# Kernel tuning notes

Measured on AMD Instinct MI355X. Metric: run time of the kernel, lower is better.

The kernel has to match this reference:

```python
import jax, jax.numpy as jnp
import numpy as np

H = 512        # hidden_dim
D_IN = 512     # input_dim
N_ACT = 16     # output_dim
DICT = 8192    # dict_len (episodic memory slots)
B = 4096       # batch
N_CYCLES = 10  # LCA iterations
DT_T = 0.6     # LCA dt/tau
EPS = 1e-8     # cosine-similarity eps


def setup_inputs() -> dict:
    key = jax.random.key(0)
    ks = jax.random.split(key, 12)
    NHT = 4 * H + 3  # (N_VSIG+1)*H + N_SSIG
    s = lambda i, shape, sc=1.0: jax.random.normal(ks[i], shape, jnp.float32) * sc
    return {
        "x_t": s(0, (1, B, D_IN)),
        "h_prev": s(1, (1, B, H), 0.1),
        "c_prev": s(2, (1, B, H), 0.1),
        "W_i2h": s(3, (NHT, D_IN), 1.0 / np.sqrt(D_IN)),
        "b_i2h": jnp.zeros((NHT,), jnp.float32),
        "W_h2h": s(4, (NHT, H), 1.0 / np.sqrt(H)),
        "b_h2h": jnp.zeros((NHT,), jnp.float32),
        "vals": s(5, (DICT, H), 0.1),  # episodic memory table
        "W_ih": s(6, (H, H), 1.0 / np.sqrt(H)),
        "b_ih": jnp.zeros((H,), jnp.float32),
        "W_actor": s(7, (N_ACT, H), 1.0 / np.sqrt(H)),
        "b_actor": jnp.zeros((N_ACT,), jnp.float32),
        "W_critic": s(8, (1, H), 1.0 / np.sqrt(H)),
        "b_critic": jnp.zeros((1,), jnp.float32),
        "mem_ptr": 0,
    }


def _lca(sim, leak, comp, w_input):
    # Leaky competing accumulator over memory slots; sim:[B,DICT], scalars:[B,1]
    ff = w_input * sim
    def step(V, _):
        inhib = comp * (jnp.sum(V, axis=-1, keepdims=True) - V)  # lateral inhibition (excl. self)
        V = jax.nn.relu(V + DT_T * (ff - leak * V - inhib))
        return V, None
    V, _ = jax.lax.scan(step, jnp.zeros_like(sim), None, length=N_CYCLES)
    return V


def reference(x_t, h_prev, c_prev, W_i2h, b_i2h, W_h2h, b_h2h, vals,
              W_ih, b_ih, W_actor, b_actor, W_critic, b_critic, mem_ptr):
    x, h, c = x_t[0], h_prev[0], c_prev[0]  # [B, dim]
    preact = x @ W_i2h.T + b_i2h + h @ W_h2h.T + b_h2h  # [B, 4H+3]
    gates = jax.nn.sigmoid(preact[:, :3 * H])
    f_t = gates[:, :H]
    o_t = gates[:, H:2 * H]
    i_t = gates[:, 2 * H:3 * H]
    inps = jax.nn.sigmoid(preact[:, 3 * H + 0])[:, None]  # input strength (gain=1)
    leak = jax.nn.sigmoid(preact[:, 3 * H + 1])[:, None]
    comp = jax.nn.sigmoid(preact[:, 3 * H + 2])[:, None]
    c_new = jnp.tanh(preact[:, 3 * H + 3:])
    c_t = c * f_t + i_t * c_new
    # --- recall: cosine similarity vs memory, then LCA competition ---
    qn = jnp.linalg.norm(c_t, axis=-1, keepdims=True)        # [B,1]
    mn = jnp.linalg.norm(vals, axis=-1, keepdims=True)       # [DICT,1]
    sim = (c_t @ vals.T) / jnp.maximum(qn * mn.T, EPS)       # [B,DICT]
    w = _lca(sim, leak, comp, inps)                          # [B,DICT]
    m_t = w @ vals                                           # [B,H]
    cm_t = c_t + m_t
    # --- encode: ring-buffer scatter write of cm_t into memory ---
    idx = (mem_ptr + jnp.arange(B)) % DICT
    new_vals = vals.at[idx].set(cm_t)
    h_t = o_t * jnp.tanh(cm_t)
    # --- A2C head ---
    a2c_h = jax.nn.relu(h_t @ W_ih.T + b_ih)
    pi = jax.nn.softmax(a2c_h @ W_actor.T + b_actor, axis=-1)
    value = a2c_h @ W_critic.T + b_critic
    return pi, value, h_t, cm_t, m_t, new_vals
```

## Files before the change

### kernel.cpp

```cpp
#include <hip/hip_runtime.h>
#include <hip/hip_fp16.h>
#include <math.h>

#define HH    512
#define DICT  8192
#define BATCH 4096
#define NCYC  10
#define DTT   0.6f

#define BM  128
#define BKT 64

using f16x8 = __attribute__((ext_vector_type(8))) _Float16;
using f32x4 = __attribute__((ext_vector_type(4))) float;

__device__ __forceinline__ float sigmoidf_(float x) { return 1.0f / (1.0f + __expf(-x)); }

__device__ __forceinline__ float waveReduceSum(float v) {
#pragma unroll
  for (int o = 1; o < 64; o <<= 1) v += __shfl_xor(v, o);
  return v;
}

__device__ __forceinline__ void gld16(const void* g, void* l) {
  __builtin_amdgcn_global_load_lds(
      (const __attribute__((address_space(1))) void*)g,
      (__attribute__((address_space(3))) void*)l, 16, 0, 0);
}

template<int N> __device__ __forceinline__ void vmwait() {
  if constexpr (N == 8)      asm volatile("s_waitcnt vmcnt(8)" ::: "memory");
  else if constexpr (N == 6) asm volatile("s_waitcnt vmcnt(6)" ::: "memory");
  else if constexpr (N == 4) asm volatile("s_waitcnt vmcnt(4)" ::: "memory");
  else if constexpr (N == 3) asm volatile("s_waitcnt vmcnt(3)" ::: "memory");
  else                       asm volatile("s_waitcnt vmcnt(0)" ::: "memory");
  __builtin_amdgcn_sched_barrier(0);
}

__device__ __forceinline__ void blockbar() {
  asm volatile("" ::: "memory");
  __builtin_amdgcn_s_barrier();
  __builtin_amdgcn_sched_barrier(0);
}

template<int ROWS>
__device__ __forceinline__ void stage_tile(const __half* gbase, int ld, char* lds, int tid) {
  constexpr int ISS = ROWS * 8 / 256;
#pragma unroll
  for (int i = 0; i < ISS; ++i) {
    int cidx = i * 256 + tid;
    int row  = cidx >> 3;
    int slot = cidx & 7;
    int k4   = slot ^ (row & 7);
    gld16(gbase + (size_t)row * ld + k4 * 8, lds + cidx * 16);
  }
}

__device__ __forceinline__ f16x8 frag_ld(const char* lds, int row, int kchunk) {
  int slot = kchunk ^ (row & 7);
  return *(const f16x8*)(lds + row * 128 + slot * 16);
}

template<int FN>
__device__ __forceinline__ void tile_mfma(const char* As, const char* Bs,
                                          int lane, int wr, int wc, f32x4 (&acc)[4][FN]) {
  const int g = lane >> 4, r = lane & 15;
#pragma unroll
  for (int ks = 0; ks < 2; ++ks) {
    f16x8 af[4], bfr[FN];
#pragma unroll
    for (int i = 0; i < 4; ++i)
      af[i] = frag_ld(As, wr * 64 + i * 16 + r, ks * 4 + g);
#pragma unroll
    for (int j = 0; j < FN; ++j)
      bfr[j] = frag_ld(Bs, wc * (FN * 16) + j * 16 + r, ks * 4 + g);
#pragma unroll
    for (int i = 0; i < 4; ++i)
#pragma unroll
      for (int j = 0; j < FN; ++j)
        acc[i][j] = __builtin_amdgcn_mfma_f32_16x16x32_f16(af[i], bfr[j], acc[i][j], 0, 0, 0);
  }
}

template<int BN, int FN>
__device__ __forceinline__ void gemm_seg(const __half* A, int lda, const __half* B, int ldb,
                                         int m0, int n0, int K, char* lds, int tid,
                                         f32x4 (&acc)[4][FN]) {
  constexpr int ABYTES = BM * BKT * 2;
  constexpr int BBYTES = BN * BKT * 2;
  constexpr int BUF = ABYTES + BBYTES;
  constexpr int NL = (BM + BN) * 8 / 256;
  const int lane = tid & 63, wid = tid >> 6;
  const int wr = wid >> 1, wc = wid & 1;
  const int nt = K / BKT;
  const __half* Ab = A + (size_t)m0 * lda;
  const __half* Bb = B + (size_t)n0 * ldb;
  stage_tile<BM>(Ab, lda, lds, tid);
  stage_tile<BN>(Bb, ldb, lds + ABYTES, tid);
  int cur = 0;
  for (int t = 0; t < nt; ++t) {
    char* curb = lds + cur * BUF;
    if (t + 1 < nt) {
      char* nxt = lds + (cur ^ 1) * BUF;
      stage_tile<BM>(Ab + (t + 1) * BKT, lda, nxt, tid);
      stage_tile<BN>(Bb + (t + 1) * BKT, ldb, nxt + ABYTES, tid);
      vmwait<NL>();
    } else {
      vmwait<0>();
    }
    blockbar();
    tile_mfma<FN>(curb, curb + ABYTES, lane, wr, wc, acc);
    blockbar();
    cur ^= 1;
  }
}

__device__ __forceinline__ void zero_acc4(f32x4 (&a)[4][4]) {
  f32x4 z = {0.f, 0.f, 0.f, 0.f};
#pragma unroll
  for (int i = 0; i < 4; ++i)
#pragma unroll
    for (int j = 0; j < 4; ++j) a[i][j] = z;
}
__device__ __forceinline__ void zero_acc2(f32x4 (&a)[4][2]) {
  f32x4 z = {0.f, 0.f, 0.f, 0.f};
#pragma unroll
  for (int i = 0; i < 4; ++i)
#pragma unroll
    for (int j = 0; j < 2; ++j) a[i][j] = z;
}

__device__ __forceinline__ int swz32(int row, int k) {
  return k ^ (row & 3) ^ ((row >> 2) & 3);
}

template<int ROWS, int NT>
__device__ __forceinline__ void stage32(const __half* gbase, int ld, char* lds, int tid) {
  constexpr int ISS = ROWS * 4 / NT;
#pragma unroll
  for (int i = 0; i < ISS; ++i) {
    int cidx = i * NT + tid;
    int row  = cidx >> 2;
    int slot = cidx & 3;
    int k4   = swz32(row, slot);
    gld16(gbase + (size_t)row * ld + k4 * 8, lds + cidx * 16);
  }
}

__device__ __forceinline__ f16x8 frag32(const char* lds, int row, int g) {
  int slot = swz32(row, g);
  return *(const f16x8*)(lds + row * 64 + slot * 16);
}

template<int MF, int NF>
__device__ __forceinline__ void tile_mfma32(const char* As, const char* Bs,
                                            int arow0, int brow0, int lane,
                                            f32x4 (&acc)[MF][NF]) {
  const int g = lane >> 4, r = lane & 15;
  f16x8 af[MF], bf[NF];
#pragma unroll
  for (int i = 0; i < MF; ++i) af[i] = frag32(As, arow0 + i * 16 + r, g);
#pragma unroll
  for (int j = 0; j < NF; ++j) bf[j] = frag32(Bs, brow0 + j * 16 + r, g);
#pragma unroll
  for (int i = 0; i < MF; ++i)
#pragma unroll
    for (int j = 0; j < NF; ++j)
      acc[i][j] = __builtin_amdgcn_mfma_f32_16x16x32_f16(af[i], bf[j], acc[i][j], 0, 0, 0);
}

__global__ __launch_bounds__(256) void k_prep(
    const float* __restrict__ x, const float* __restrict__ h,
    const float* __restrict__ Wi, const float* __restrict__ Wh, const float* __restrict__ Wih,
    const float* __restrict__ vals, const int* __restrict__ mptr,
    __half* __restrict__ x_h, __half* __restrict__ h_h,
    __half* __restrict__ Wip_h, __half* __restrict__ Whp_h, __half* __restrict__ Wih_h,
    float* __restrict__ nv, __half* __restrict__ vals_h, float* __restrict__ rmn,
    __half* __restrict__ vT) {
  __shared__ float tile[32][33];
  const int bid = blockIdx.x;
  if (bid < 6400) {
    int gq = bid * 256 + threadIdx.x;
    const float* src; __half* dst; int si, di;
    if (gq < 524288) {
      src = x; dst = x_h; si = di = gq * 4;
    } else if (gq < 1048576) {
      src = h; dst = h_h; si = di = (gq - 524288) * 4;
    } else if (gq < 1310720) {
      int iq = gq - 1048576;
      int jp = iq >> 7, k4 = (iq & 127) << 2;
      int U = jp >> 6, g = (jp >> 4) & 3, r = jp & 15;
      int u = U * 16 + r;
      int orig = g * 512 + u + (g == 3 ? 3 : 0);
      src = Wi; dst = Wip_h; si = orig * 512 + k4; di = jp * 512 + k4;
    } else if (gq < 1572864) {
      int iq = gq - 1310720;
      int jp = iq >> 7, k4 = (iq & 127) << 2;
      int U = jp >> 6, g = (jp >> 4) & 3, r = jp & 15;
      int u = U * 16 + r;
      int orig = g * 512 + u + (g == 3 ? 3 : 0);
      src = Wh; dst = Whp_h; si = orig * 512 + k4; di = jp * 512 + k4;
    } else if (gq < 1638400) {
      int iq = gq - 1572864;
      src = Wih; dst = Wih_h; si = di = iq * 4;
    } else return;
    float4 v = *(const float4*)(src + si);
    *(__half2*)(dst + di)     = __floats2half2_rn(v.x, v.y);
    *(__half2*)(dst + di + 2) = __floats2half2_rn(v.z, v.w);
  } else if (bid < 8448) {
    const int row  = (bid - 6400) * 4 + (threadIdx.x >> 6);
    const int lane = threadIdx.x & 63;
    const float* vr = vals + (size_t)row * HH + lane * 8;
    float4 a = *(const float4*)(vr);
    float4 b = *(const float4*)(vr + 4);
    if (((row + DICT - mptr[0]) & (DICT - 1)) >= BATCH) {
      float* nvp = nv + (size_t)row * HH + lane * 8;
      *(float4*)(nvp)     = a;
      *(float4*)(nvp + 4) = b;
    }
    __half* vh = vals_h + (size_t)row * HH + lane * 8;
    *(__half2*)(vh)     = __floats2half2_rn(a.x, a.y);
    *(__half2*)(vh + 2) = __floats2half2_rn(a.z, a.w);
    *(__half2*)(vh + 4) = __floats2half2_rn(b.x, b.y);
    *(__half2*)(vh + 6) = __floats2half2_rn(b.z, b.w);
    float ss = a.x * a.x + a.y * a.y + a.z * a.z + a.w * a.w
             + b.x * b.x + b.y * b.y + b.z * b.z + b.w * b.w;
    ss = waveReduceSum(ss);
    if (lane == 0) rmn[row] = 1.f / fmaxf(sqrtf(ss), 1e-12f);
  } else {
    const int idx = bid - 8448;
    const int r0 = (idx & 255) * 32, c0 = (idx >> 8) * 32;
    const int tr = threadIdx.x >> 5, tc = threadIdx.x & 31;
#pragma unroll
    for (int p = 0; p < 4; ++p)
      tile[tr + p * 8][tc] = vals[(size_t)(r0 + tr + p * 8) * HH + c0 + tc];
    __syncthreads();
#pragma unroll
    for (int p = 0; p < 4; ++p)
      vT[(size_t)(c0 + tr + p * 8) * DICT + r0 + tc] = __float2half(tile[tc][tr + p * 8]);
  }
}

__global__ __launch_bounds__(256) void k_preact(
    const __half* __restrict__ x_h, const __half* __restrict__ h_h,
    const __half* __restrict__ Wip, const __half* __restrict__ Whp,
    const float* __restrict__ bi, const float* __restrict__ bh,
    const float* __restrict__ c_prev,
    float* __restrict__ ct, float* __restrict__ ot, __half* __restrict__ ct_h) {
  __shared__ char smem[2 * (BM * BKT * 2 + 128 * BKT * 2)] __attribute__((aligned(16)));
  const int tid = threadIdx.x;
  const int m0 = blockIdx.y * 128, n0 = blockIdx.x * 128;
  f32x4 acc[4][4]; zero_acc4(acc);
  gemm_seg<128, 4>(x_h, HH, Wip, HH, m0, n0, HH, smem, tid, acc);
  gemm_seg<128, 4>(h_h, HH, Whp, HH, m0, n0, HH, smem, tid, acc);
  const int lane = tid & 63, wid = tid >> 6, wr = wid >> 1, wc = wid & 1;
  const int r = lane & 15;
  const int u = ((n0 >> 6) + wc) * 16 + r;
  float bsum[4];
#pragma unroll
  for (int g = 0; g < 4; ++g) {
    int orig = g * 512 + u + (g == 3 ? 3 : 0);
    bsum[g] = bi[orig] + bh[orig];
  }
#pragma unroll
  for (int fi = 0; fi < 4; ++fi)
#pragma unroll
    for (int q = 0; q < 4; ++q) {
      int m = m0 + wr * 64 + fi * 16 + (lane >> 4) * 4 + q;
      float f  = sigmoidf_(acc[fi][0][q] + bsum[0]);
      float o  = sigmoidf_(acc[fi][1][q] + bsum[1]);
      float ii = sigmoidf_(acc[fi][2][q] + bsum[2]);
      float cn = tanhf(acc[fi][3][q] + bsum[3]);
      size_t off = (size_t)m * HH + u;
      float cc = c_prev[off] * f + ii * cn;
      ct[off] = cc; ot[off] = o; ct_h[off] = __float2half(cc);
    }
}

__global__ __launch_bounds__(256) void k_scalars(
    const float* __restrict__ x, const float* __restrict__ h,
    const float* __restrict__ Wi, const float* __restrict__ Wh,
    const float* __restrict__ bi, const float* __restrict__ bh,
    const float* __restrict__ ct,
    float* __restrict__ inps, float* __restrict__ leak,
    float* __restrict__ comp, float* __restrict__ rqn) {
  const int b = blockIdx.x, wid = threadIdx.x >> 6, lane = threadIdx.x & 63;
  const int j = lane * 8;
  if (wid < 3) {
    const float* wi = Wi + (size_t)(1536 + wid) * HH + j;
    const float* wh = Wh + (size_t)(1536 + wid) * HH + j;
    const float* xr = x + (size_t)b * HH + j;
    const float* hr = h + (size_t)b * HH + j;
    float4 xa = *(const float4*)(xr), xb = *(const float4*)(xr + 4);
    float4 wa = *(const float4*)(wi), wb = *(const float4*)(wi + 4);
    float4 ha = *(const float4*)(hr), hb = *(const float4*)(hr + 4);
    float4 va = *(const float4*)(wh), vb = *(const float4*)(wh + 4);
    float s = xa.x * wa.x + xa.y * wa.y + xa.z * wa.z + xa.w * wa.w
            + xb.x * wb.x + xb.y * wb.y + xb.z * wb.z + xb.w * wb.w
            + ha.x * va.x + ha.y * va.y + ha.z * va.z + ha.w * va.w
            + hb.x * vb.x + hb.y * vb.y + hb.z * vb.z + hb.w * vb.w;
    s = waveReduceSum(s);
    if (lane == 0) {
      float v = sigmoidf_(s + bi[1536 + wid] + bh[1536 + wid]);
      if (wid == 0) inps[b] = v; else if (wid == 1) leak[b] = v; else comp[b] = v;
    }
  } else {
    const float* cr = ct + (size_t)b * HH + j;
    float4 a = *(const float4*)(cr), d = *(const float4*)(cr + 4);
    float ss = a.x * a.x + a.y * a.y + a.z * a.z + a.w * a.w
             + d.x * d.x + d.y * d.y + d.z * d.z + d.w * d.w;
    ss = waveReduceSum(ss);
    if (lane == 0) rqn[b] = 1.f / fmaxf(sqrtf(ss), 1e-12f);
  }
}

__global__ __launch_bounds__(512, 2) void k_sim(
    const __half* __restrict__ ct_h, const __half* __restrict__ vals_h,
    const float* __restrict__ rqn, const float* __restrict__ rmn,
    __half* __restrict__ sim_h) {
  __shared__ char smem[65536] __attribute__((aligned(16)));
  const int tid = threadIdx.x, lane = tid & 63, wid = tid >> 6;
  const int wr = wid >> 2, wc = wid & 3;
  const int bid = blockIdx.x;
  const int xcd = bid & 7, idx = bid >> 3;
  const int m0 = (xcd * 2 + (idx & 1)) * 256;
  const int n0 = (idx >> 1) * 256;
  f32x4 acc[8][4];
  { f32x4 z = {0.f, 0.f, 0.f, 0.f};
#pragma unroll
    for (int i = 0; i < 8; ++i)
#pragma unroll
      for (int j = 0; j < 4; ++j) acc[i][j] = z; }
  const __half* Ab = ct_h + (size_t)m0 * HH;
  const __half* Bb = vals_h + (size_t)n0 * HH;
  stage32<256, 512>(Ab, HH, smem, tid);
  stage32<256, 512>(Bb, HH, smem + 16384, tid);
  int cur = 0;
  for (int t = 0; t < 16; ++t) {
    char* curb = smem + cur * 32768;
    if (t < 15) {
      char* nxt = smem + (cur ^ 1) * 32768;
      stage32<256, 512>(Ab + (t + 1) * 32, HH, nxt, tid);
      stage32<256, 512>(Bb + (t + 1) * 32, HH, nxt + 16384, tid);
      vmwait<4>();
    } else {
      vmwait<0>();
    }
    blockbar();
    __builtin_amdgcn_s_setprio(1);
    tile_mfma32<8, 4>(curb, curb + 16384, wr * 128, wc * 64, lane, acc);
    __builtin_amdgcn_s_setprio(0);
    blockbar();
    cur ^= 1;
  }
  float* T = (float*)smem;
  const int g = lane >> 4, r = lane & 15;
  const int lrow = tid >> 4, seg = (tid & 15) * 16;
  float rmv[16];
  *(float4*)(rmv)      = *(const float4*)(rmn + n0 + seg);
  *(float4*)(rmv + 4)  = *(const float4*)(rmn + n0 + seg + 4);
  *(float4*)(rmv + 8)  = *(const float4*)(rmn + n0 + seg + 8);
  *(float4*)(rmv + 12) = *(const float4*)(rmn + n0 + seg + 12);
#pragma unroll
  for (int fi = 0; fi < 8; ++fi) {
    if (fi) __syncthreads();
#pragma unroll
    for (int fj = 0; fj < 4; ++fj)
#pragma unroll
      for (int q = 0; q < 4; ++q)
        T[(wr * 16 + g * 4 + q) * 260 + wc * 64 + fj * 16 + r] = acc[fi][fj][q];
    __syncthreads();
    int m = m0 + (lrow >> 4) * 128 + fi * 16 + (lrow & 15);
    float rq = rqn[m];
    const float* Tr = T + lrow * 260 + seg;
    f16x8 o0, o1;
#pragma unroll
    for (int j = 0; j < 8; ++j) o0[j] = (_Float16)(Tr[j] * rq * rmv[j]);
#pragma unroll
    for (int j = 0; j < 8; ++j) o1[j] = (_Float16)(Tr[8 + j] * rq * rmv[8 + j]);
    *(f16x8*)(sim_h + (size_t)m * DICT + n0 + seg)     = o0;
    *(f16x8*)(sim_h + (size_t)m * DICT + n0 + seg + 8) = o1;
  }
}

__global__ __launch_bounds__(256) void k_lca(
    const __half* __restrict__ sim_h, const float* __restrict__ inps,
    const float* __restrict__ leak, const float* __restrict__ comp,
    __half* __restrict__ w_h) {
  const int b = blockIdx.x, t = threadIdx.x;
  const __half* srow = sim_h + (size_t)b * DICT + t * 32;
  const float ffs = DTT * inps[b];
  const float a   = 1.0f - DTT * leak[b] + DTT * comp[b];
  const float cdt = DTT * comp[b];
  float ff[32], V[32];
#pragma unroll
  for (int i = 0; i < 4; ++i) {
    f16x8 v8 = *(const f16x8*)(srow + i * 8);
#pragma unroll
    for (int j = 0; j < 8; ++j) { ff[i * 8 + j] = ffs * (float)v8[j]; V[i * 8 + j] = 0.f; }
  }
  __shared__ float ps[4];
  for (int it = 0; it < NCYC; ++it) {
    float s = 0.f;
#pragma unroll
    for (int i = 0; i < 32; ++i) s += V[i];
    s = waveReduceSum(s);
    if ((t & 63) == 0) ps[t >> 6] = s;
    __syncthreads();
    float S = ps[0] + ps[1] + ps[2] + ps[3];
    __syncthreads();
    float sub = cdt * S;
#pragma unroll
    for (int i = 0; i < 32; ++i) V[i] = fmaxf(fmaf(a, V[i], ff[i] - sub), 0.f);
  }
  __half* wrow = w_h + (size_t)b * DICT + t * 32;
#pragma unroll
  for (int i = 0; i < 4; ++i) {
    f16x8 o8;
#pragma unroll
    for (int j = 0; j < 8; ++j) o8[j] = (_Float16)V[i * 8 + j];
    *(f16x8*)(wrow + i * 8) = o8;
  }
}

__global__ __launch_bounds__(512, 2) void k_mt_p(
    const __half* __restrict__ w_h, const __half* __restrict__ vT_h,
    float* __restrict__ partial) {
  __shared__ char smem[49152] __attribute__((aligned(16)));
  const int tid = threadIdx.x, lane = tid & 63, wid = tid >> 6;
  const int wr = wid >> 1, wc = wid & 1;
  const int bid = blockIdx.x;
  const int xcd = bid & 7, idx = bid >> 3;
  const int s = xcd >> 1, sub = xcd & 1;
  const int n = idx >> 3, mq = idx & 7;
  const int m0 = (mq * 2 + sub) * 256, n0 = n * 128;
  f32x4 acc[4][4]; zero_acc4(acc);
  const __half* Ab = w_h + (size_t)m0 * DICT + s * 2048;
  const __half* Bb = vT_h + (size_t)n0 * DICT + s * 2048;
  stage32<256, 512>(Ab, DICT, smem, tid);
  stage32<128, 512>(Bb, DICT, smem + 16384, tid);
  int cur = 0;
  for (int t = 0; t < 64; ++t) {
    char* curb = smem + cur * 24576;
    if (t < 63) {
      char* nxt = smem + (cur ^ 1) * 24576;
      stage32<256, 512>(Ab + (t + 1) * 32, DICT, nxt, tid);
      stage32<128, 512>(Bb + (t + 1) * 32, DICT, nxt + 16384, tid);
      vmwait<3>();
    } else {
      vmwait<0>();
    }
    blockbar();
    __builtin_amdgcn_s_setprio(1);
    tile_mfma32<4, 4>(curb, curb + 16384, wr * 64, wc * 64, lane, acc);
    __builtin_amdgcn_s_setprio(0);
    blockbar();
    cur ^= 1;
  }
  float* T = (float*)smem;
  const int g = lane >> 4, r = lane & 15;
  const int lrow = tid >> 3, seg = (tid & 7) * 16;
  float* pbase = partial + (size_t)s * (BATCH * HH);
#pragma unroll
  for (int fi = 0; fi < 4; ++fi) {
    if (fi) __syncthreads();
#pragma unroll
    for (int fj = 0; fj < 4; ++fj)
#pragma unroll
      for (int q = 0; q < 4; ++q)
        T[(wr * 16 + g * 4 + q) * 132 + wc * 64 + fj * 16 + r] = acc[fi][fj][q];
    __syncthreads();
    int mm = m0 + (lrow >> 4) * 64 + fi * 16 + (lrow & 15);
    const float* Tr = T + lrow * 132 + seg;
    float* dst = pbase + (size_t)mm * HH + n0 + seg;
    *(float4*)(dst)      = *(const float4*)(Tr);
    *(float4*)(dst + 4)  = *(const float4*)(Tr + 4);
    *(float4*)(dst + 8)  = *(const float4*)(Tr + 8);
    *(float4*)(dst + 12) = *(const float4*)(Tr + 12);
  }
}

__global__ __launch_bounds__(256) void k_mt_red(
    const float* __restrict__ partial,
    const float* __restrict__ ct, const float* __restrict__ ot, const int* __restrict__ mptr,
    float* __restrict__ out_mt, float* __restrict__ out_cmt, float* __restrict__ out_ht,
    float* __restrict__ out_nv, __half* __restrict__ ht_h) {
  const int i4 = blockIdx.x * 256 + threadIdx.x;
  const size_t off = (size_t)i4 * 4;
  const int m = i4 >> 7;
  float4 p  = *(const float4*)(partial + off);
  float4 p1 = *(const float4*)(partial + 2097152 + off);
  float4 p2 = *(const float4*)(partial + 4194304 + off);
  float4 p3 = *(const float4*)(partial + 6291456 + off);
  p.x += p1.x + p2.x + p3.x;
  p.y += p1.y + p2.y + p3.y;
  p.z += p1.z + p2.z + p3.z;
  p.w += p1.w + p2.w + p3.w;
  float4 c4 = *(const float4*)(ct + off);
  float4 o4 = *(const float4*)(ot + off);
  float4 cm, hv;
  cm.x = c4.x + p.x; hv.x = o4.x * tanhf(cm.x);
  cm.y = c4.y + p.y; hv.y = o4.y * tanhf(cm.y);
  cm.z = c4.z + p.z; hv.z = o4.z * tanhf(cm.z);
  cm.w = c4.w + p.w; hv.w = o4.w * tanhf(cm.w);
  *(float4*)(out_mt + off)  = p;
  *(float4*)(out_cmt + off) = cm;
  *(float4*)(out_ht + off)  = hv;
  *(__half2*)(ht_h + off)     = __floats2half2_rn(hv.x, hv.y);
  *(__half2*)(ht_h + off + 2) = __floats2half2_rn(hv.z, hv.w);
  const int nvrow = (mptr[0] + m) & (DICT - 1);
  *(float4*)(out_nv + (size_t)nvrow * HH + (off & 511)) = cm;
}

__global__ __launch_bounds__(256) void k_a2c(
    const __half* __restrict__ ht_h, const __half* __restrict__ Wih_h,
    const float* __restrict__ bih, float* __restrict__ a2c) {
  __shared__ char smem[2 * (BM * BKT * 2 + 64 * BKT * 2)] __attribute__((aligned(16)));
  const int tid = threadIdx.x;
  const int bid = blockIdx.x;
  const int xn = (bid >> 3) & 7, ym = (bid & 7) | ((bid >> 6) << 3);
  const int m0 = ym * 128, n0 = xn * 64;
  f32x4 acc[4][2]; zero_acc2(acc);
  gemm_seg<64, 2>(ht_h, HH, Wih_h, HH, m0, n0, HH, smem, tid, acc);
  const int lane = tid & 63, wid = tid >> 6, wr = wid >> 1, wc = wid & 1;
  float* T = (float*)smem;
  const int gg = lane >> 4, r = lane & 15;
  const int lrow = tid >> 3, c8 = (tid & 7) * 8;
  float4 b0 = *(const float4*)(bih + n0 + c8);
  float4 b1 = *(const float4*)(bih + n0 + c8 + 4);
#pragma unroll
  for (int fi = 0; fi < 4; ++fi) {
    if (fi) __syncthreads();
#pragma unroll
    for (int fj = 0; fj < 2; ++fj)
#pragma unroll
      for (int qq = 0; qq < 4; ++qq)
        T[(wr * 16 + gg * 4 + qq) * 68 + wc * 32 + fj * 16 + r] = acc[fi][fj][qq];
    __syncthreads();
    int mm = m0 + (lrow >> 4) * 64 + fi * 16 + (lrow & 15);
    float4 v0 = *(const float4*)(T + lrow * 68 + c8);
    float4 v1 = *(const float4*)(T + lrow * 68 + c8 + 4);
    v0.x = fmaxf(v0.x + b0.x, 0.f); v0.y = fmaxf(v0.y + b0.y, 0.f);
    v0.z = fmaxf(v0.z + b0.z, 0.f); v0.w = fmaxf(v0.w + b0.w, 0.f);
    v1.x = fmaxf(v1.x + b1.x, 0.f); v1.y = fmaxf(v1.y + b1.y, 0.f);
    v1.z = fmaxf(v1.z + b1.z, 0.f); v1.w = fmaxf(v1.w + b1.w, 0.f);
    float* dst = a2c + (size_t)mm * HH + n0 + c8;
    *(float4*)dst       = v0;
    *(float4*)(dst + 4) = v1;
  }
}

__global__ __launch_bounds__(256) void k_actor(
    const float* __restrict__ a2c,
    const float* __restrict__ Wact, const float* __restrict__ bact,
    const float* __restrict__ Wcr, const float* __restrict__ bcr,
    float* __restrict__ out_pi, float* __restrict__ out_val) {
  const int b = blockIdx.x * 4 + (threadIdx.x >> 6);
  const int lane = threadIdx.x & 63;
  const float* hrow = a2c + (size_t)b * HH;
  float4 a0 = *(const float4*)(hrow + (lane << 3));
  float4 a1 = *(const float4*)(hrow + (lane << 3) + 4);
  float lg[17];
#pragma unroll
  for (int o = 0; o < 17; ++o) {
    const float* wr = (o < 16) ? (Wact + (size_t)o * HH) : Wcr;
    float4 w0 = *(const float4*)(wr + (lane << 3));
    float4 w1 = *(const float4*)(wr + (lane << 3) + 4);
    float s = a0.x * w0.x + a0.y * w0.y + a0.z * w0.z + a0.w * w0.w
            + a1.x * w1.x + a1.y * w1.y + a1.z * w1.z + a1.w * w1.w;
    lg[o] = waveReduceSum(s);
  }
#pragma unroll
  for (int o = 0; o < 16; ++o) lg[o] += bact[o];
  float mx = lg[0];
#pragma unroll
  for (int o = 1; o < 16; ++o) mx = fmaxf(mx, lg[o]);
  float e[16], sum = 0.f;
#pragma unroll
  for (int o = 0; o < 16; ++o) { e[o] = __expf(lg[o] - mx); sum += e[o]; }
  float rs = 1.f / sum;
  if (lane == 0) {
#pragma unroll
    for (int o = 0; o < 16; ++o) out_pi[(size_t)b * 16 + o] = e[o] * rs;
    out_val[b] = lg[16] + bcr[0];
  }
}

extern "C" void kernel_launch(void* const* d_in, const int* in_sizes, int n_in,
                              void* d_out, int out_size, void* d_ws, size_t ws_size,
                              hipStream_t stream) {
  const float* x    = (const float*)d_in[0];
  const float* h    = (const float*)d_in[1];
  const float* c    = (const float*)d_in[2];
  const float* Wi   = (const float*)d_in[3];
  const float* bi   = (const float*)d_in[4];
  const float* Wh   = (const float*)d_in[5];
  const float* bh   = (const float*)d_in[6];
  const float* vals = (const float*)d_in[7];
  const float* Wih  = (const float*)d_in[8];
  const float* bih  = (const float*)d_in[9];
  const float* Wact = (const float*)d_in[10];
  const float* bact = (const float*)d_in[11];
  const float* Wcr  = (const float*)d_in[12];
  const float* bcr  = (const float*)d_in[13];
  const int*   mptr = (const int*)d_in[14];

  float* F = (float*)d_ws;
  __half* w_h    = (__half*)F;
  __half* sim_h   = (__half*)(F + 16777216);
  float*  a2c     = F + 16777216;
  float*  partial = F + 33554432;
  float*  ct     = F + 50331648;
  float*  ot     = F + 52428800;
  __half* ct_h   = (__half*)(F + 54525952);
  __half* vals_h = (__half*)(F + 55574528);
  __half* vT_h   = (__half*)(F + 57671680);
  __half* x_h    = (__half*)(F + 59768832);
  __half* ht_h   = x_h;
  __half* h_h    = (__half*)(F + 60817408);
  __half* Wip_h  = (__half*)(F + 61865984);
  __half* Whp_h  = (__half*)(F + 62423040);
  __half* Wih_h  = (__half*)(F + 62980096);
  float*  inps   = F + 63111168;
  float*  leak   = inps + 4096;
  float*  comp   = leak + 4096;
  float*  rqn    = comp + 4096;
  float*  rmn    = rqn + 4096;

  float* out     = (float*)d_out;
  float* out_pi  = out;
  float* out_val = out + 65536;
  float* out_ht  = out + 69632;
  float* out_cmt = out_ht + 2097152;
  float* out_mt  = out_cmt + 2097152;
  float* out_nv  = out_mt + 2097152;

  dim3 b256(256);
  dim3 b512(512);
  k_prep   <<<12544, b256, 0, stream>>>(x, h, Wi, Wh, Wih, vals, mptr,
                                        x_h, h_h, Wip_h, Whp_h, Wih_h,
                                        out_nv, vals_h, rmn, vT_h);
  k_preact <<<dim3(16, 32), b256, 0, stream>>>(x_h, h_h, Wip_h, Whp_h, bi, bh, c,
                                               ct, ot, ct_h);
  k_scalars<<<BATCH, b256, 0, stream>>>(x, h, Wi, Wh, bi, bh, ct, inps, leak, comp, rqn);
  k_sim    <<<512, b512, 0, stream>>>(ct_h, vals_h, rqn, rmn, sim_h);
  k_lca    <<<BATCH, b256, 0, stream>>>(sim_h, inps, leak, comp, w_h);
  k_mt_p   <<<256, b512, 0, stream>>>(w_h, vT_h, partial);
  k_mt_red <<<2048, b256, 0, stream>>>(partial, ct, ot, mptr,
                                       out_mt, out_cmt, out_ht, out_nv, ht_h);
  k_a2c    <<<256, b256, 0, stream>>>(ht_h, Wih_h, bih, a2c);
  k_actor  <<<BATCH / 4, b256, 0, stream>>>(a2c, Wact, bact, Wcr, bcr, out_pi, out_val);
}
```

Before: 235.9 us.

## Switch LDS layout to paired-row 128B lines and split m_t GEMM 8-way in K

The shared-memory staging layout changes from 64-byte rows with an XOR swizzle to 128-byte lines that pack two rows (row and row+HALF) with an 8-slot XOR swizzle, which is meant to reduce LDS bank conflicts on fragment reads. The w@vals GEMM kernel is re-split from a 4-way K split over 256 blocks to an 8-way K split over 512 blocks, for more parallelism and better CU occupancy. The reduction kernel now sums 8 partial buffers instead of 4, which doubles partial-buffer traffic and needs the partial allocation to hold 8 slices; XCD-aware block mapping is dropped.

```diff
diff --git a/kernel.cpp b/kernel.cpp
--- a/kernel.cpp
+++ b/kernel.cpp
@@ -130,38 +130,40 @@
     for (int j = 0; j < 2; ++j) a[i][j] = z;
 }
 
-__device__ __forceinline__ int swz32(int row, int k) {
-  return k ^ (row & 3) ^ ((row >> 2) & 3);
-}
-
 template<int ROWS, int NT>
 __device__ __forceinline__ void stage32(const __half* gbase, int ld, char* lds, int tid) {
+  constexpr int HALF = ROWS / 2;
   constexpr int ISS = ROWS * 4 / NT;
 #pragma unroll
   for (int i = 0; i < ISS; ++i) {
     int cidx = i * NT + tid;
-    int row  = cidx >> 2;
-    int slot = cidx & 3;
-    int k4   = swz32(row, slot);
+    int line = cidx >> 3;
+    int slot = cidx & 7;
+    int t    = slot ^ (line & 7);
+    int row  = line + HALF * (t >> 2);
+    int k4   = t & 3;
     gld16(gbase + (size_t)row * ld + k4 * 8, lds + cidx * 16);
   }
 }
 
+template<int HALF>
 __device__ __forceinline__ f16x8 frag32(const char* lds, int row, int g) {
-  int slot = swz32(row, g);
-  return *(const f16x8*)(lds + row * 64 + slot * 16);
-}
-
-template<int MF, int NF>
+  int line = row & (HALF - 1);
+  int t    = g + 4 * (row / HALF);
+  int slot = t ^ (line & 7);
+  return *(const f16x8*)(lds + line * 128 + slot * 16);
+}
+
+template<int MF, int NF, int AHALF, int BHALF>
 __device__ __forceinline__ void tile_mfma32(const char* As, const char* Bs,
                                             int arow0, int brow0, int lane,
                                             f32x4 (&acc)[MF][NF]) {
   const int g = lane >> 4, r = lane & 15;
   f16x8 af[MF], bf[NF];
 #pragma unroll
-  for (int i = 0; i < MF; ++i) af[i] = frag32(As, arow0 + i * 16 + r, g);
-#pragma unroll
-  for (int j = 0; j < NF; ++j) bf[j] = frag32(Bs, brow0 + j * 16 + r, g);
+  for (int i = 0; i < MF; ++i) af[i] = frag32<AHALF>(As, arow0 + i * 16 + r, g);
+#pragma unroll
+  for (int j = 0; j < NF; ++j) bf[j] = frag32<BHALF>(Bs, brow0 + j * 16 + r, g);
 #pragma unroll
   for (int i = 0; i < MF; ++i)
 #pragma unroll
@@ -348,7 +350,7 @@
     }
     blockbar();
     __builtin_amdgcn_s_setprio(1);
-    tile_mfma32<8, 4>(curb, curb + 16384, wr * 128, wc * 64, lane, acc);
+    tile_mfma32<8, 4, 128, 128>(curb, curb + 16384, wr * 128, wc * 64, lane, acc);
     __builtin_amdgcn_s_setprio(0);
     blockbar();
     cur ^= 1;
@@ -430,19 +432,18 @@
   const int tid = threadIdx.x, lane = tid & 63, wid = tid >> 6;
   const int wr = wid >> 1, wc = wid & 1;
   const int bid = blockIdx.x;
-  const int xcd = bid & 7, idx = bid >> 3;
-  const int s = xcd >> 1, sub = xcd & 1;
-  const int n = idx >> 3, mq = idx & 7;
-  const int m0 = (mq * 2 + sub) * 256, n0 = n * 128;
+  const int s = bid & 7, idx = bid >> 3;
+  const int n = idx & 3, m = idx >> 2;
+  const int m0 = m * 256, n0 = n * 128;
   f32x4 acc[4][4]; zero_acc4(acc);
-  const __half* Ab = w_h + (size_t)m0 * DICT + s * 2048;
-  const __half* Bb = vT_h + (size_t)n0 * DICT + s * 2048;
+  const __half* Ab = w_h + (size_t)m0 * DICT + s * 1024;
+  const __half* Bb = vT_h + (size_t)n0 * DICT + s * 1024;
   stage32<256, 512>(Ab, DICT, smem, tid);
   stage32<128, 512>(Bb, DICT, smem + 16384, tid);
   int cur = 0;
-  for (int t = 0; t < 64; ++t) {
+  for (int t = 0; t < 32; ++t) {
     char* curb = smem + cur * 24576;
-    if (t < 63) {
+    if (t < 31) {
       char* nxt = smem + (cur ^ 1) * 24576;
       stage32<256, 512>(Ab + (t + 1) * 32, DICT, nxt, tid);
       stage32<128, 512>(Bb + (t + 1) * 32, DICT, nxt + 16384, tid);
@@ -452,7 +453,7 @@
     }
     blockbar();
     __builtin_amdgcn_s_setprio(1);
-    tile_mfma32<4, 4>(curb, curb + 16384, wr * 64, wc * 64, lane, acc);
+    tile_mfma32<4, 4, 128, 64>(curb, curb + 16384, wr * 64, wc * 64, lane, acc);
     __builtin_amdgcn_s_setprio(0);
     blockbar();
     cur ^= 1;
@@ -488,14 +489,12 @@
   const int i4 = blockIdx.x * 256 + threadIdx.x;
   const size_t off = (size_t)i4 * 4;
   const int m = i4 >> 7;
-  float4 p  = *(const float4*)(partial + off);
-  float4 p1 = *(const float4*)(partial + 2097152 + off);
-  float4 p2 = *(const float4*)(partial + 4194304 + off);
-  float4 p3 = *(const float4*)(partial + 6291456 + off);
-  p.x += p1.x + p2.x + p3.x;
-  p.y += p1.y + p2.y + p3.y;
-  p.z += p1.z + p2.z + p3.z;
-  p.w += p1.w + p2.w + p3.w;
+  float4 p = *(const float4*)(partial + off);
+#pragma unroll
+  for (int s = 1; s < 8; ++s) {
+    float4 q = *(const float4*)(partial + (size_t)s * 2097152 + off);
+    p.x += q.x; p.y += q.y; p.z += q.z; p.w += q.w;
+  }
   float4 c4 = *(const float4*)(ct + off);
   float4 o4 = *(const float4*)(ot + off);
   float4 cm, hv;
@@ -645,7 +644,7 @@
   k_scalars<<<BATCH, b256, 0, stream>>>(x, h, Wi, Wh, bi, bh, ct, inps, leak, comp, rqn);
   k_sim    <<<512, b512, 0, stream>>>(ct_h, vals_h, rqn, rmn, sim_h);
   k_lca    <<<BATCH, b256, 0, stream>>>(sim_h, inps, leak, comp, w_h);
-  k_mt_p   <<<256, b512, 0, stream>>>(w_h, vT_h, partial);
+  k_mt_p   <<<512, b512, 0, stream>>>(w_h, vT_h, partial);
   k_mt_red <<<2048, b256, 0, stream>>>(partial, ct, ot, mptr,
                                        out_mt, out_cmt, out_ht, out_nv, ht_h);
   k_a2c    <<<256, b256, 0, stream>>>(ht_h, Wih_h, bih, a2c);
```

Result: slower. 241.1 us (+2.2%).
